# Performance work log

Measured on AMD Instinct MI355X. Metric: run time of the kernel, lower is better.

## Reference

```python
import jax, jax.numpy as jnp
import numpy as np
from jax import lax

B, T, D, H = 64, 512, 512, 512


def setup_inputs() -> dict:
    key = jax.random.key(0)
    k1, k2, k3, k4 = jax.random.split(key, 4)
    inputs = jax.random.normal(k1, (B, T, D), dtype=jnp.float32)
    lengths = jax.random.randint(k2, (B,), 1, T + 1, dtype=jnp.int32)
    c0 = jnp.zeros((B, H), dtype=jnp.float32)
    h0 = jnp.zeros((B, H), dtype=jnp.float32)
    scale_i = 1.0 / np.sqrt(D)
    scale_h = 1.0 / np.sqrt(H)
    Wi = jax.random.normal(k3, (D, 4 * H), dtype=jnp.float32) * scale_i
    Wh = jax.random.normal(k4, (H, 4 * H), dtype=jnp.float32) * scale_h
    b = jnp.zeros((4 * H,), dtype=jnp.float32)
    return {"inputs": inputs, "lengths": lengths, "c0": c0, "h0": h0,
            "Wi": Wi, "Wh": Wh, "b": b, "reverse": 1}


def _flip_sequences(seq, lengths):
    # seq: [B, T, F]; keeps padding at the end while flipping valid prefix.
    t = seq.shape[1]
    idxs = (jnp.arange(t - 1, -1, -1)[None, :] + lengths[:, None]) % t  # [B, T]
    return jnp.take_along_axis(seq, idxs[:, :, None], axis=1)


def reference(inputs, lengths, c0, h0, Wi, Wh, b, reverse):
    batch, t, _ = inputs.shape
    if reverse:
        inputs = _flip_sequences(inputs, lengths)

    def step(carry, x_t):
        c, h = carry
        z = x_t @ Wi + h @ Wh + b  # [B, 4H]
        i_g, f_g, g_g, o_g = jnp.split(z, 4, axis=-1)
        c_new = jax.nn.sigmoid(f_g) * c + jax.nn.sigmoid(i_g) * jnp.tanh(g_g)
        h_new = jax.nn.sigmoid(o_g) * jnp.tanh(c_new)
        return (c_new, h_new), (c_new, h_new)

    xs = jnp.swapaxes(inputs, 0, 1)  # [T, B, D]
    _, (cs, hs) = lax.scan(step, (c0, h0), xs)
    cs = jnp.swapaxes(cs, 0, 1)  # [B, T, H]
    hs = jnp.swapaxes(hs, 0, 1)  # [B, T, H]
    outputs = hs

    last = lengths - 1
    bidx = jnp.arange(batch)
    c_final = cs[bidx, last]
    h_final = hs[bidx, last]

    if reverse:
        outputs = _flip_sequences(outputs, lengths)
    return outputs, (c_final, h_final)
```

## Files before the change

kernel.cpp:

```cpp
#include <hip/hip_runtime.h>

#define B_ 64
#define T_ 512
#define D_ 512
#define H_ 512
#define NG 2048

typedef __attribute__((ext_vector_type(8))) short short8;
typedef __attribute__((ext_vector_type(4))) float floatx4;
typedef __attribute__((ext_vector_type(4))) unsigned int uintx4;

static __device__ __forceinline__ unsigned short f2bf(float f) {
    unsigned int u = __float_as_uint(f);
    return (unsigned short)((u + 0x7FFFu + ((u >> 16) & 1u)) >> 16);
}

static __device__ __forceinline__ short8 pack8(float4 a, float4 b) {
    short8 r;
    r[0] = (short)f2bf(a.x); r[1] = (short)f2bf(a.y);
    r[2] = (short)f2bf(a.z); r[3] = (short)f2bf(a.w);
    r[4] = (short)f2bf(b.x); r[5] = (short)f2bf(b.y);
    r[6] = (short)f2bf(b.z); r[7] = (short)f2bf(b.w);
    return r;
}

static __device__ __forceinline__ float sigm(float x) { return 1.0f / (1.0f + __expf(-x)); }
static __device__ __forceinline__ float tanh_(float x) {
    float e = __expf(2.0f * x);
    return 1.0f - 2.0f / (e + 1.0f);
}

__global__ __launch_bounds__(256) void transpose_w(
    const float* __restrict__ Wi, const float* __restrict__ Wh,
    unsigned short* __restrict__ WiT, unsigned short* __restrict__ WhT)
{
    __shared__ float tile[64][65];
    const float* src = blockIdx.z ? Wh : Wi;
    unsigned short* dst = blockIdx.z ? WhT : WiT;
    const int n0 = blockIdx.x * 64, k0 = blockIdx.y * 64;
    const int cx = threadIdx.x & 63, ry = threadIdx.x >> 6;
#pragma unroll
    for (int i = 0; i < 16; ++i) {
        int k = ry * 16 + i;
        tile[k][cx] = src[(size_t)(k0 + k) * NG + n0 + cx];
    }
    __syncthreads();
#pragma unroll
    for (int i = 0; i < 16; ++i) {
        int n = ry * 16 + i;
        dst[(size_t)(n0 + n) * D_ + k0 + cx] = f2bf(tile[cx][n]);
    }
}

__global__ __launch_bounds__(256) void zx_gemm(
    const float* __restrict__ x, const int* __restrict__ lengths,
    const unsigned short* __restrict__ WiT, const float* __restrict__ bias,
    const int* __restrict__ revp, _Float16* __restrict__ zx)
{
    __shared__ unsigned short a_lds[128][40];
    __shared__ unsigned short b_lds[128][40];

    const int mt = blockIdx.x, nt = blockIdx.y;
    const int tid = threadIdx.x;
    const int lane = tid & 63, w = tid >> 6;
    const int wm = w & 1, wn = w >> 1;

    const int b = mt >> 2;
    const int len = lengths[b];
    const int rev = revp[0];

    const int r = tid >> 1;
    const int kh = (tid & 1) << 4;
    const int t = ((mt & 3) << 7) + r;
    const int src_t = rev ? ((T_ - 1 - t + len) & (T_ - 1)) : t;
    const float* arow = x + ((size_t)b * T_ + src_t) * D_;
    const unsigned short* brow = WiT + (size_t)(nt * 128 + r) * D_;

    floatx4 acc[4][4];
#pragma unroll
    for (int i = 0; i < 4; ++i)
#pragma unroll
        for (int j = 0; j < 4; ++j) acc[i][j] = (floatx4){0.f, 0.f, 0.f, 0.f};

    for (int kt = 0; kt < D_ / 32; ++kt) {
        const float4* ap = (const float4*)(arow + kt * 32 + kh);
        float4 a0 = ap[0], a1 = ap[1], a2 = ap[2], a3 = ap[3];
        const uint4* bp = (const uint4*)(brow + kt * 32 + kh);
        uint4 bq0 = bp[0], bq1 = bp[1];
        *(short8*)&a_lds[r][kh]     = pack8(a0, a1);
        *(short8*)&a_lds[r][kh + 8] = pack8(a2, a3);
        *(uint4*)&b_lds[r][kh]     = bq0;
        *(uint4*)&b_lds[r][kh + 8] = bq1;
        __syncthreads();

        short8 af[4], bfr[4];
#pragma unroll
        for (int mi = 0; mi < 4; ++mi)
            af[mi] = *(const short8*)&a_lds[wm * 64 + mi * 16 + (lane & 15)][(lane >> 4) << 3];
#pragma unroll
        for (int ni = 0; ni < 4; ++ni)
            bfr[ni] = *(const short8*)&b_lds[wn * 64 + ni * 16 + (lane & 15)][(lane >> 4) << 3];
#pragma unroll
        for (int mi = 0; mi < 4; ++mi)
#pragma unroll
            for (int ni = 0; ni < 4; ++ni)
                acc[mi][ni] = __builtin_amdgcn_mfma_f32_16x16x32_bf16(af[mi], bfr[ni], acc[mi][ni], 0, 0, 0);
        __syncthreads();
    }

#pragma unroll
    for (int mi = 0; mi < 4; ++mi) {
#pragma unroll
        for (int ni = 0; ni < 4; ++ni) {
            int row = wm * 64 + mi * 16 + ((lane >> 4) << 2);
            int col = nt * 128 + wn * 64 + ni * 16 + (lane & 15);
            float bv = bias[col];
            size_t base = (size_t)(mt * 128 + row) * NG + col;
#pragma unroll
            for (int v = 0; v < 4; ++v)
                zx[base + (size_t)v * NG] = (_Float16)(acc[mi][ni][v] + bv);
        }
    }
}

__global__ __launch_bounds__(256, 1) void lstm_rec(
    const _Float16* __restrict__ zx, const unsigned short* __restrict__ WhT,
    const float* __restrict__ c0, const float* __restrict__ h0,
    const int* __restrict__ lengths, const int* __restrict__ revp,
    float* __restrict__ out, unsigned short* __restrict__ h_data,
    unsigned int* __restrict__ sent)
{
    __shared__ unsigned short h_lds[16][520];

    const int bid = blockIdx.x;
    const int gb = bid & 3, gh = bid >> 2;
    const int tid = threadIdx.x;
    const int lane = tid & 63, w = tid >> 6;
    const int b0 = gb * 16, u0 = gh * 32;
    const int rev = revp[0];

    const int colh = lane & 15;
    const int rr = (lane >> 4) << 2;
    const int cg = colh >> 3;
    const int cu = colh & 7;
    const int uu = w * 8 + cu;
    const int khw = (lane >> 4) << 3;

    int len_v[4]; float c[4];
#pragma unroll
    for (int v = 0; v < 4; ++v) {
        len_v[v] = lengths[b0 + rr + v];
        c[v] = c0[(size_t)(b0 + rr + v) * H_ + u0 + uu];
    }

    short8 bw[16][2];
#pragma unroll
    for (int ni = 0; ni < 2; ++ni) {
        const unsigned short* src = WhT + (size_t)((ni * 2 + cg) * H_ + u0 + uu) * D_ + khw;
#pragma unroll
        for (int kk = 0; kk < 16; ++kk)
            bw[kk][ni] = *(const short8*)(src + kk * 32);
    }

    float zxv[2][4];
#pragma unroll
    for (int ni = 0; ni < 2; ++ni)
#pragma unroll
        for (int v = 0; v < 4; ++v)
            zxv[ni][v] = (float)zx[((size_t)(b0 + rr + v) * T_) * NG + (ni * 2 + cg) * H_ + u0 + uu];

    const int sr2 = tid & 15;
    const int ph  = tid >> 4;
    const int scc = ph * 32;

    for (int s = 0; s < T_; ++s) {
        if (s == 0) {
            const float* hp = h0 + (size_t)(b0 + sr2) * H_ + scc;
#pragma unroll
            for (int q = 0; q < 4; ++q) {
                float4 f0 = *(const float4*)(hp + q * 8);
                float4 f1 = *(const float4*)(hp + q * 8 + 4);
                *(short8*)&h_lds[sr2][scc + q * 8] = pack8(f0, f1);
            }
        } else {
            const unsigned int* sentp = sent + ((size_t)(s & 1) * 4 + gb) * 16 + ph;
            for (;;) {
                unsigned int sv;
                asm volatile("global_load_dword %0, %1, off sc0 sc1\n\t"
                             "s_waitcnt vmcnt(0)"
                             : "=v"(sv) : "v"(sentp) : "memory");
                if (sv == (unsigned int)s) break;
                __builtin_amdgcn_s_sleep(1);
            }
            const unsigned short* dp = h_data + ((size_t)(s & 1) * B_ + b0 + sr2) * H_ + scc;
            uintx4 q0, q1;
            asm volatile("global_load_dwordx4 %0, %2, off sc0 sc1\n\t"
                         "global_load_dwordx4 %1, %3, off sc0 sc1\n\t"
                         "s_waitcnt vmcnt(0)"
                         : "=&v"(q0), "=&v"(q1)
                         : "v"(dp), "v"(dp + 8) : "memory");
            *(uintx4*)&h_lds[sr2][scc]     = q0;
            *(uintx4*)&h_lds[sr2][scc + 8] = q1;
            asm volatile("global_load_dwordx4 %0, %2, off sc0 sc1\n\t"
                         "global_load_dwordx4 %1, %3, off sc0 sc1\n\t"
                         "s_waitcnt vmcnt(0)"
                         : "=&v"(q0), "=&v"(q1)
                         : "v"(dp + 16), "v"(dp + 24) : "memory");
            *(uintx4*)&h_lds[sr2][scc + 16] = q0;
            *(uintx4*)&h_lds[sr2][scc + 24] = q1;
        }
        __syncthreads();

        floatx4 acc[2];
        acc[0] = (floatx4){0.f, 0.f, 0.f, 0.f};
        acc[1] = (floatx4){0.f, 0.f, 0.f, 0.f};
#pragma unroll
        for (int kk = 0; kk < 16; ++kk) {
            short8 af = *(const short8*)&h_lds[lane & 15][kk * 32 + khw];
            acc[0] = __builtin_amdgcn_mfma_f32_16x16x32_bf16(af, bw[kk][0], acc[0], 0, 0, 0);
            acc[1] = __builtin_amdgcn_mfma_f32_16x16x32_bf16(af, bw[kk][1], acc[1], 0, 0, 0);
        }

        float hn_v[4], cn_v[4];
#pragma unroll
        for (int v = 0; v < 4; ++v) {
            float own0 = acc[0][v] + zxv[0][v];
            float own1 = acc[1][v] + zxv[1][v];
            float oth0 = __shfl_xor(own0, 8);
            float oth1 = __shfl_xor(own1, 8);
            float zi = cg ? oth0 : own0;
            float zf = cg ? own0 : oth0;
            float zg = cg ? oth1 : own1;
            float zo = cg ? own1 : oth1;
            float ig = sigm(zi), fg = sigm(zf);
            float gg = tanh_(zg), og = sigm(zo);
            float cn = fg * c[v] + ig * gg;
            float hn = og * tanh_(cn);
            c[v] = cn; cn_v[v] = cn; hn_v[v] = hn;
            if (cg == 1 && s + 1 < T_) {
                unsigned short* dst =
                    h_data + ((size_t)((s + 1) & 1) * B_ + b0 + rr + v) * H_ + u0 + uu;
                unsigned int val = (unsigned int)f2bf(hn);
                asm volatile("global_store_short %0, %1, off sc0 sc1"
                             :: "v"(dst), "v"(val) : "memory");
            }
        }
#pragma unroll
        for (int v = 0; v < 4; ++v) {
            const int b = b0 + rr + v;
            const int ug = u0 + uu;
            int orig_t = rev ? ((T_ - 1 - s + len_v[v]) & (T_ - 1)) : s;
            if (cg == 0)
                out[((size_t)b * T_ + orig_t) * H_ + ug] = hn_v[v];
            if (s == len_v[v] - 1) {
                size_t fin = (size_t)B_ * T_ * H_;
                if (cg == 0) out[fin + (size_t)b * H_ + ug] = cn_v[v];
                else         out[fin + (size_t)B_ * H_ + (size_t)b * H_ + ug] = hn_v[v];
            }
        }

        __syncthreads();

        if (s + 1 < T_) {
            if (tid == 0) {
                unsigned int* sp2 = sent + ((size_t)((s + 1) & 1) * 4 + gb) * 16 + gh;
                unsigned int sval = (unsigned int)(s + 1);
                asm volatile("global_store_dword %0, %1, off sc0 sc1"
                             :: "v"(sp2), "v"(sval) : "memory");
            }
#pragma unroll
            for (int ni = 0; ni < 2; ++ni)
#pragma unroll
                for (int v = 0; v < 4; ++v)
                    zxv[ni][v] = (float)zx[((size_t)(b0 + rr + v) * T_ + s + 1) * NG +
                                           (ni * 2 + cg) * H_ + u0 + uu];
        }
    }
}

extern "C" void kernel_launch(void* const* d_in, const int* in_sizes, int n_in,
                              void* d_out, int out_size, void* d_ws, size_t ws_size,
                              hipStream_t stream)
{
    const float* x       = (const float*)d_in[0];
    const int*   lengths = (const int*)d_in[1];
    const float* c0      = (const float*)d_in[2];
    const float* h0      = (const float*)d_in[3];
    const float* Wi      = (const float*)d_in[4];
    const float* Wh      = (const float*)d_in[5];
    const float* bias    = (const float*)d_in[6];
    const int*   revp    = (const int*)d_in[7];
    float* out = (float*)d_out;

    char* ws = (char*)d_ws;
    const size_t OFF_WIT = 0;
    const size_t OFF_WHT = 2ull << 20;
    const size_t OFF_ZX  = 4ull << 20;
    const size_t OFF_HD  = OFF_ZX + (size_t)B_ * T_ * NG * 2;
    const size_t HD_BYTES = 2ull * B_ * H_ * 2;
    const size_t OFF_SENT = OFF_HD + HD_BYTES;
    const size_t SENT_BYTES = 2ull * 4 * 16 * 4;
    const size_t NEED = OFF_SENT + SENT_BYTES;
    if (ws_size < NEED) return;

    unsigned short* WiT = (unsigned short*)(ws + OFF_WIT);
    unsigned short* WhT = (unsigned short*)(ws + OFF_WHT);
    _Float16* zx        = (_Float16*)(ws + OFF_ZX);
    unsigned short* h_data = (unsigned short*)(ws + OFF_HD);
    unsigned int* sent  = (unsigned int*)(ws + OFF_SENT);

    hipMemsetAsync(sent, 0, SENT_BYTES, stream);
    dim3 gt(32, 8, 2);
    transpose_w<<<gt, 256, 0, stream>>>(Wi, Wh, WiT, WhT);
    dim3 g1(256, 16);
    zx_gemm<<<g1, 256, 0, stream>>>(x, lengths, WiT, bias, revp, zx);
    lstm_rec<<<64, 256, 0, stream>>>(zx, WhT, c0, h0, lengths, revp, out, h_data, sent);
}
```

Baseline: 1.784 ms.

## Stage new h in LDS and publish with vector stores before signaling

Each block now gathers its freshly computed h slice into a small LDS buffer. One wavefront then publishes it to global memory with coalesced 16-byte stores, replacing many scattered 2-byte stores, and raises the step flag immediately afterward. This moves the cross-block signal ahead of the output writes and the next zx prefetch, so the critical path between timesteps is shorter. The four h-read loads are also issued together under a single wait. It adds an extra __syncthreads, and the flag store depends on the s_waitcnt ordering to make the h data visible before the flag.

```diff
diff --git a/kernel.cpp b/kernel.cpp
--- a/kernel.cpp
+++ b/kernel.cpp
@@ -131,6 +131,7 @@
     unsigned int* __restrict__ sent)
 {
     __shared__ unsigned short h_lds[16][520];
+    __shared__ unsigned short h_next[16][32];
 
     const int bid = blockIdx.x;
     const int gb = bid & 3, gh = bid >> 2;
@@ -172,6 +173,14 @@
     const int sr2 = tid & 15;
     const int ph  = tid >> 4;
     const int scc = ph * 32;
+
+    const int pbb = lane >> 2, pq = lane & 3;
+    unsigned short* pub_base[2];
+    pub_base[0] = h_data + ((size_t)0 * B_ + b0 + pbb) * H_ + u0 + pq * 8;
+    pub_base[1] = h_data + ((size_t)1 * B_ + b0 + pbb) * H_ + u0 + pq * 8;
+    unsigned int* sent_w[2];
+    sent_w[0] = sent + (0 * 4 + gb) * 16 + gh;
+    sent_w[1] = sent + (1 * 4 + gb) * 16 + gh;
 
     for (int s = 0; s < T_; ++s) {
         if (s == 0) {
@@ -193,21 +202,19 @@
                 __builtin_amdgcn_s_sleep(1);
             }
             const unsigned short* dp = h_data + ((size_t)(s & 1) * B_ + b0 + sr2) * H_ + scc;
-            uintx4 q0, q1;
-            asm volatile("global_load_dwordx4 %0, %2, off sc0 sc1\n\t"
-                         "global_load_dwordx4 %1, %3, off sc0 sc1\n\t"
+            uintx4 q0, q1, q2, q3;
+            asm volatile("global_load_dwordx4 %0, %4, off sc0 sc1\n\t"
+                         "global_load_dwordx4 %1, %5, off sc0 sc1\n\t"
+                         "global_load_dwordx4 %2, %6, off sc0 sc1\n\t"
+                         "global_load_dwordx4 %3, %7, off sc0 sc1\n\t"
                          "s_waitcnt vmcnt(0)"
-                         : "=&v"(q0), "=&v"(q1)
-                         : "v"(dp), "v"(dp + 8) : "memory");
-            *(uintx4*)&h_lds[sr2][scc]     = q0;
-            *(uintx4*)&h_lds[sr2][scc + 8] = q1;
-            asm volatile("global_load_dwordx4 %0, %2, off sc0 sc1\n\t"
-                         "global_load_dwordx4 %1, %3, off sc0 sc1\n\t"
-                         "s_waitcnt vmcnt(0)"
-                         : "=&v"(q0), "=&v"(q1)
-                         : "v"(dp + 16), "v"(dp + 24) : "memory");
-            *(uintx4*)&h_lds[sr2][scc + 16] = q0;
-            *(uintx4*)&h_lds[sr2][scc + 24] = q1;
+                         : "=&v"(q0), "=&v"(q1), "=&v"(q2), "=&v"(q3)
+                         : "v"(dp), "v"(dp + 8), "v"(dp + 16), "v"(dp + 24)
+                         : "memory");
+            *(uintx4*)&h_lds[sr2][scc]      = q0;
+            *(uintx4*)&h_lds[sr2][scc + 8]  = q1;
+            *(uintx4*)&h_lds[sr2][scc + 16] = q2;
+            *(uintx4*)&h_lds[sr2][scc + 24] = q3;
         }
         __syncthreads();
 
@@ -237,14 +244,24 @@
             float cn = fg * c[v] + ig * gg;
             float hn = og * tanh_(cn);
             c[v] = cn; cn_v[v] = cn; hn_v[v] = hn;
-            if (cg == 1 && s + 1 < T_) {
-                unsigned short* dst =
-                    h_data + ((size_t)((s + 1) & 1) * B_ + b0 + rr + v) * H_ + u0 + uu;
-                unsigned int val = (unsigned int)f2bf(hn);
-                asm volatile("global_store_short %0, %1, off sc0 sc1"
-                             :: "v"(dst), "v"(val) : "memory");
+            if (cg == 1)
+                h_next[rr + v][uu] = f2bf(hn);
+        }
+        __syncthreads();
+
+        if (w == 0 && s + 1 < T_) {
+            uintx4 pv = *(const uintx4*)&h_next[pbb][pq * 8];
+            unsigned short* dst = pub_base[(s + 1) & 1];
+            asm volatile("global_store_dwordx4 %0, %1, off sc0 sc1\n\t"
+                         "s_waitcnt vmcnt(0)"
+                         :: "v"(dst), "v"(pv) : "memory");
+            if (lane == 0) {
+                unsigned int sval = (unsigned int)(s + 1);
+                asm volatile("global_store_dword %0, %1, off sc0 sc1"
+                             :: "v"(sent_w[(s + 1) & 1]), "v"(sval) : "memory");
             }
         }
+
 #pragma unroll
         for (int v = 0; v < 4; ++v) {
             const int b = b0 + rr + v;
@@ -258,16 +275,7 @@
                 else         out[fin + (size_t)B_ * H_ + (size_t)b * H_ + ug] = hn_v[v];
             }
         }
-
-        __syncthreads();
-
         if (s + 1 < T_) {
-            if (tid == 0) {
-                unsigned int* sp2 = sent + ((size_t)((s + 1) & 1) * 4 + gb) * 16 + gh;
-                unsigned int sval = (unsigned int)(s + 1);
-                asm volatile("global_store_dword %0, %1, off sc0 sc1"
-                             :: "v"(sp2), "v"(sval) : "memory");
-            }
 #pragma unroll
             for (int ni = 0; ni < 2; ++ni)
 #pragma unroll
```

Measured after the change: 1.849 ms. 1.04x slower.

## Embed step tags with hidden-state data to replace separate flag handshake

Applied to the files above, without the earlier changes.

Each 16-byte chunk of the exchanged hidden state now carries its step number, so consumers poll the data directly instead of waiting on a separate sent flag and then loading the data. Producers gather h into LDS and write tagged 16-byte chunks with single vector stores, which removes a barrier-then-flag round trip per step. In exchange, the volume exchanged per step doubles because of the tag padding, and an extra LDS staging barrier is added. Correctness relies on each 16-byte store becoming visible atomically.

```diff
diff --git a/kernel.cpp b/kernel.cpp
--- a/kernel.cpp
+++ b/kernel.cpp
@@ -127,10 +127,10 @@
     const _Float16* __restrict__ zx, const unsigned short* __restrict__ WhT,
     const float* __restrict__ c0, const float* __restrict__ h0,
     const int* __restrict__ lengths, const int* __restrict__ revp,
-    float* __restrict__ out, unsigned short* __restrict__ h_data,
-    unsigned int* __restrict__ sent)
+    float* __restrict__ out, unsigned int* __restrict__ hx)
 {
     __shared__ unsigned short h_lds[16][520];
+    __shared__ unsigned short h_next[16][32];
 
     const int bid = blockIdx.x;
     const int gb = bid & 3, gh = bid >> 2;
@@ -172,6 +172,9 @@
     const int sr2 = tid & 15;
     const int ph  = tid >> 4;
     const int scc = ph * 32;
+    const int probeq = (sr2 + ph) & 7;
+
+    const int L = (w << 6) | lane;
 
     for (int s = 0; s < T_; ++s) {
         if (s == 0) {
@@ -183,31 +186,45 @@
                 *(short8*)&h_lds[sr2][scc + q * 8] = pack8(f0, f1);
             }
         } else {
-            const unsigned int* sentp = sent + ((size_t)(s & 1) * 4 + gb) * 16 + ph;
+            const unsigned int* dp = hx + ((((unsigned)(s & 1) * 4 + gb) * 16 + ph) << 9) + (sr2 << 5);
+            uintx4 k0, k1, k2, k3, k4, k5, k6, k7;
             for (;;) {
-                unsigned int sv;
-                asm volatile("global_load_dword %0, %1, off sc0 sc1\n\t"
-                             "s_waitcnt vmcnt(0)"
-                             : "=v"(sv) : "v"(sentp) : "memory");
-                if (sv == (unsigned int)s) break;
-                __builtin_amdgcn_s_sleep(1);
+                asm volatile(
+                    "global_load_dwordx4 %0, %8, off sc0 sc1\n\t"
+                    "global_load_dwordx4 %1, %8, off offset:16 sc0 sc1\n\t"
+                    "global_load_dwordx4 %2, %8, off offset:32 sc0 sc1\n\t"
+                    "global_load_dwordx4 %3, %8, off offset:48 sc0 sc1\n\t"
+                    "global_load_dwordx4 %4, %8, off offset:64 sc0 sc1\n\t"
+                    "global_load_dwordx4 %5, %8, off offset:80 sc0 sc1\n\t"
+                    "global_load_dwordx4 %6, %8, off offset:96 sc0 sc1\n\t"
+                    "global_load_dwordx4 %7, %8, off offset:112 sc0 sc1\n\t"
+                    "s_waitcnt vmcnt(0)"
+                    : "=&v"(k0), "=&v"(k1), "=&v"(k2), "=&v"(k3),
+                      "=&v"(k4), "=&v"(k5), "=&v"(k6), "=&v"(k7)
+                    : "v"(dp) : "memory");
+                const unsigned int tg = (unsigned int)s;
+                bool ok = (k0[2] == tg) & (k1[2] == tg) & (k2[2] == tg) & (k3[2] == tg) &
+                          (k4[2] == tg) & (k5[2] == tg) & (k6[2] == tg) & (k7[2] == tg);
+                if (ok) break;
+                const unsigned int* pp = dp + (probeq << 2) + 2;
+                for (;;) {
+                    unsigned int tv;
+                    asm volatile("global_load_dword %0, %1, off sc0 sc1\n\t"
+                                 "s_waitcnt vmcnt(0)"
+                                 : "=v"(tv) : "v"(pp) : "memory");
+                    if (tv == tg) break;
+                    __builtin_amdgcn_s_sleep(1);
+                }
             }
-            const unsigned short* dp = h_data + ((size_t)(s & 1) * B_ + b0 + sr2) * H_ + scc;
-            uintx4 q0, q1;
-            asm volatile("global_load_dwordx4 %0, %2, off sc0 sc1\n\t"
-                         "global_load_dwordx4 %1, %3, off sc0 sc1\n\t"
-                         "s_waitcnt vmcnt(0)"
-                         : "=&v"(q0), "=&v"(q1)
-                         : "v"(dp), "v"(dp + 8) : "memory");
-            *(uintx4*)&h_lds[sr2][scc]     = q0;
-            *(uintx4*)&h_lds[sr2][scc + 8] = q1;
-            asm volatile("global_load_dwordx4 %0, %2, off sc0 sc1\n\t"
-                         "global_load_dwordx4 %1, %3, off sc0 sc1\n\t"
-                         "s_waitcnt vmcnt(0)"
-                         : "=&v"(q0), "=&v"(q1)
-                         : "v"(dp + 16), "v"(dp + 24) : "memory");
-            *(uintx4*)&h_lds[sr2][scc + 16] = q0;
-            *(uintx4*)&h_lds[sr2][scc + 24] = q1;
+            uintx4 e;
+            e[0] = k0[0]; e[1] = k0[1]; e[2] = k1[0]; e[3] = k1[1];
+            *(uintx4*)&h_lds[sr2][scc]      = e;
+            e[0] = k2[0]; e[1] = k2[1]; e[2] = k3[0]; e[3] = k3[1];
+            *(uintx4*)&h_lds[sr2][scc + 8]  = e;
+            e[0] = k4[0]; e[1] = k4[1]; e[2] = k5[0]; e[3] = k5[1];
+            *(uintx4*)&h_lds[sr2][scc + 16] = e;
+            e[0] = k6[0]; e[1] = k6[1]; e[2] = k7[0]; e[3] = k7[1];
+            *(uintx4*)&h_lds[sr2][scc + 24] = e;
         }
         __syncthreads();
 
@@ -237,14 +254,21 @@
             float cn = fg * c[v] + ig * gg;
             float hn = og * tanh_(cn);
             c[v] = cn; cn_v[v] = cn; hn_v[v] = hn;
-            if (cg == 1 && s + 1 < T_) {
-                unsigned short* dst =
-                    h_data + ((size_t)((s + 1) & 1) * B_ + b0 + rr + v) * H_ + u0 + uu;
-                unsigned int val = (unsigned int)f2bf(hn);
-                asm volatile("global_store_short %0, %1, off sc0 sc1"
-                             :: "v"(dst), "v"(val) : "memory");
-            }
-        }
+            if (cg == 1)
+                h_next[rr + v][uu] = f2bf(hn);
+        }
+        __syncthreads();
+
+        if (L < 128 && s + 1 < T_) {
+            const int pb = L >> 3, pu = (L & 7) << 2;
+            uint2 hv = *(const uint2*)&h_next[pb][pu];
+            uintx4 ck;
+            ck[0] = hv.x; ck[1] = hv.y; ck[2] = (unsigned int)(s + 1); ck[3] = 0u;
+            unsigned int* dst = hx + ((((unsigned)((s + 1) & 1) * 4 + gb) * 16 + gh) << 9) + (L << 2);
+            asm volatile("global_store_dwordx4 %0, %1, off sc0 sc1"
+                         :: "v"(dst), "v"(ck) : "memory");
+        }
+
 #pragma unroll
         for (int v = 0; v < 4; ++v) {
             const int b = b0 + rr + v;
@@ -258,16 +282,7 @@
                 else         out[fin + (size_t)B_ * H_ + (size_t)b * H_ + ug] = hn_v[v];
             }
         }
-
-        __syncthreads();
-
         if (s + 1 < T_) {
-            if (tid == 0) {
-                unsigned int* sp2 = sent + ((size_t)((s + 1) & 1) * 4 + gb) * 16 + gh;
-                unsigned int sval = (unsigned int)(s + 1);
-                asm volatile("global_store_dword %0, %1, off sc0 sc1"
-                             :: "v"(sp2), "v"(sval) : "memory");
-            }
 #pragma unroll
             for (int ni = 0; ni < 2; ++ni)
 #pragma unroll
@@ -296,23 +311,20 @@
     const size_t OFF_WIT = 0;
     const size_t OFF_WHT = 2ull << 20;
     const size_t OFF_ZX  = 4ull << 20;
-    const size_t OFF_HD  = OFF_ZX + (size_t)B_ * T_ * NG * 2;
-    const size_t HD_BYTES = 2ull * B_ * H_ * 2;
-    const size_t OFF_SENT = OFF_HD + HD_BYTES;
-    const size_t SENT_BYTES = 2ull * 4 * 16 * 4;
-    const size_t NEED = OFF_SENT + SENT_BYTES;
+    const size_t OFF_HX  = OFF_ZX + (size_t)B_ * T_ * NG * 2;
+    const size_t HX_BYTES = 2ull * 4 * 16 * 128 * 16;
+    const size_t NEED = OFF_HX + HX_BYTES;
     if (ws_size < NEED) return;
 
     unsigned short* WiT = (unsigned short*)(ws + OFF_WIT);
     unsigned short* WhT = (unsigned short*)(ws + OFF_WHT);
     _Float16* zx        = (_Float16*)(ws + OFF_ZX);
-    unsigned short* h_data = (unsigned short*)(ws + OFF_HD);
-    unsigned int* sent  = (unsigned int*)(ws + OFF_SENT);
-
-    hipMemsetAsync(sent, 0, SENT_BYTES, stream);
+    unsigned int* hx    = (unsigned int*)(ws + OFF_HX);
+
+    hipMemsetAsync(hx, 0, HX_BYTES, stream);
     dim3 gt(32, 8, 2);
     transpose_w<<<gt, 256, 0, stream>>>(Wi, Wh, WiT, WhT);
     dim3 g1(256, 16);
     zx_gemm<<<g1, 256, 0, stream>>>(x, lengths, WiT, bias, revp, zx);
-    lstm_rec<<<64, 256, 0, stream>>>(zx, WhT, c0, h0, lengths, revp, out, h_data, sent);
-}
+    lstm_rec<<<64, 256, 0, stream>>>(zx, WhT, c0, h0, lengths, revp, out, hx);
+}
```

Measured after the change: 1.888 ms. 5.9% more time.
